# Optimization experiments

Measured on AMD Instinct MI355X. Metric: run time of the kernel, lower is better.

## Reference

```python
import jax, jax.numpy as jnp
import numpy as np

B, T, D, H = 64, 512, 1024, 1024


def setup_inputs() -> dict:
    key = jax.random.key(0)
    k1, k2, k3, k4, k5 = jax.random.split(key, 5)
    return {
        "c0": jax.random.normal(k1, (B, H), jnp.float32),
        "h0": jax.random.normal(k2, (B, H), jnp.float32),
        "x": jax.random.normal(k3, (B, T, D), jnp.float32),
        "Wi": jax.random.normal(k4, (D, 4 * H), jnp.float32) * 0.02,
        "Wh": jax.random.normal(k5, (H, 4 * H), jnp.float32) * 0.02,
        "b": jnp.zeros((4 * H,), jnp.float32),
    }


def reference(c0, h0, x, Wi, Wh, b):
    # flax OptimizedLSTMCell: fused gates = x @ Wi (no bias) + h @ Wh + b,
    # split into i, f, g, o; carry = (c, h).
    def step(carry, xt):
        c, h = carry
        gates = xt @ Wi + h @ Wh + b  # [B, 4H]
        i, f, g, o = jnp.split(gates, 4, axis=-1)
        new_c = jax.nn.sigmoid(f) * c + jax.nn.sigmoid(i) * jnp.tanh(g)
        new_h = jax.nn.sigmoid(o) * jnp.tanh(new_c)
        return (new_c, new_h), new_h

    # scan over time axis (original uses in_axes=1/out_axes=1)
    (cT, hT), ys = jax.lax.scan(step, (c0, h0), jnp.swapaxes(x, 0, 1))
    return cT, hT, jnp.swapaxes(ys, 0, 1)  # final carry + [B, T, H] outputs
```

## Files before the change

### kernel.cpp

```cpp
#include <hip/hip_runtime.h>

#define B_ 64
#define T_ 512
#define D_ 1024
#define H_ 1024
#define NG_ 4096

typedef __attribute__((ext_vector_type(8))) short short8v;
typedef __attribute__((ext_vector_type(4))) float f32x4;

static __device__ inline unsigned short f2bf(float f) {
  unsigned u = __float_as_uint(f);
  return (unsigned short)((u + 0x7fffu + ((u >> 16) & 1u)) >> 16);
}
static __device__ inline float bf2f(unsigned short s) {
  return __uint_as_float((unsigned)s << 16);
}

static __device__ inline float4 llc_load4(const float* p) {
  float4 r;
  asm volatile("global_load_dwordx4 %0, %1, off sc0 sc1" : "=v"(r) : "v"(p));
  return r;
}
static __device__ inline void llc_store1(float* p, float v) {
  asm volatile("global_store_dword %0, %1, off sc0 sc1" :: "v"(p), "v"(v) : "memory");
}
static __device__ inline void llc_store_u16(unsigned short* p, unsigned v) {
  asm volatile("global_store_short %0, %1, off sc0 sc1" :: "v"(p), "v"(v) : "memory");
}
#define VMWAIT(N)                                          \
  asm volatile("s_waitcnt vmcnt(" #N ")" ::: "memory");    \
  __builtin_amdgcn_sched_barrier(0);

__global__ __launch_bounds__(256) void k_trans_h_fwd(const float* __restrict__ h,
                                                     float* __restrict__ hT) {
  int idx = blockIdx.x * 256 + threadIdx.x;
  int b = idx & 63;
  int k = idx >> 6;
  hT[idx] = h[b * H_ + k];
}
__global__ __launch_bounds__(256) void k_trans_h_back(const float* __restrict__ hT,
                                                      float* __restrict__ h) {
  int idx = blockIdx.x * 256 + threadIdx.x;
  int k = idx & (H_ - 1);
  int b = idx >> 10;
  h[idx] = hT[k * 64 + b];
}

__global__ __launch_bounds__(256) void k_init_hfrag(const float* __restrict__ h0,
                                                    unsigned short* __restrict__ hf) {
  const int idx = blockIdx.x * 256 + threadIdx.x;
  const int j = idx & 7;
  const int l = (idx >> 3) & 63;
  const int bt = (idx >> 9) & 3;
  const int kt = idx >> 11;
  const int b = bt * 16 + (l & 15);
  const int k = kt * 32 + ((l >> 4) << 3) + j;
  hf[idx] = f2bf(h0[b * H_ + k]);
}

__global__ __launch_bounds__(256) void k_h_final(const float* __restrict__ ys,
                                                 float* __restrict__ h) {
  const int idx = blockIdx.x * 256 + threadIdx.x;
  const int b = idx >> 10;
  const int k = idx & 1023;
  h[idx] = ys[(size_t)b * (T_ * H_) + (size_t)(T_ - 1) * H_ + k];
}

__global__ __launch_bounds__(256) void k_prep_w(const float* __restrict__ Wi,
                                                short8v* __restrict__ wh,
                                                short8v* __restrict__ wl) {
  const int idx = blockIdx.x * 256 + threadIdx.x;
  const int l = idx & 63;
  const int kt = (idx >> 6) & 31;
  const int nt = idx >> 11;
  const int n = nt * 16 + (l & 15);
  const int k = kt * 32 + ((l >> 4) << 3);
  short8v h, lo;
#pragma unroll
  for (int j = 0; j < 8; ++j) {
    const float v = Wi[(size_t)(k + j) * NG_ + n];
    const unsigned short bh = f2bf(v);
    h[j] = (short)bh;
    lo[j] = (short)f2bf(v - bf2f(bh));
  }
  wh[idx] = h;
  wl[idx] = lo;
}

__global__ __launch_bounds__(256) void k_prep_x(const float* __restrict__ x,
                                                short8v* __restrict__ xh,
                                                short8v* __restrict__ xl,
                                                int t0) {
  const int idx = blockIdx.x * 256 + threadIdx.x;
  const int l = idx & 63;
  const int bt = (idx >> 6) & 3;
  const int kt = (idx >> 8) & 31;
  const int tt = idx >> 13;
  const int b = bt * 16 + (l & 15);
  const int k = kt * 32 + ((l >> 4) << 3);
  const float* p = x + ((size_t)b * T_ + (t0 + tt)) * D_ + k;
  const float4 f0 = *(const float4*)p;
  const float4 f1 = *(const float4*)(p + 4);
  const float v[8] = {f0.x, f0.y, f0.z, f0.w, f1.x, f1.y, f1.z, f1.w};
  short8v h, lo;
#pragma unroll
  for (int j = 0; j < 8; ++j) {
    const unsigned short bh = f2bf(v[j]);
    h[j] = (short)bh;
    lo[j] = (short)f2bf(v[j] - bf2f(bh));
  }
  xh[idx] = h;
  xl[idx] = lo;
}

__global__ __launch_bounds__(512, 2) void k_fused(
    const float* __restrict__ Wh,
    const short8v* __restrict__ xh, const short8v* __restrict__ xl,
    const short8v* __restrict__ wh, const short8v* __restrict__ wl,
    const float* __restrict__ bias,
    float* __restrict__ gx,
    unsigned short* __restrict__ hfA, unsigned short* __restrict__ hfB,
    float* __restrict__ c_state,
    float* __restrict__ ys,
    unsigned* __restrict__ bar,
    int t0, int tc) {
  extern __shared__ char smemc[];

  const int tid = threadIdx.x;
  const int l = tid & 63;
  const int w = tid >> 6;
  const int bid = blockIdx.x;
  unsigned* done = bar + 512;

  if (bid >= 128) {
    const int gi = bid - 128;
    const int oct = gi & 7;
    const int nt0 = oct * 32 + w * 4;
    for (int j = gi; j < tc * 8; j += 128) {
      const int tt = j >> 3;
      f32x4 acc[4][4];
#pragma unroll
      for (int i = 0; i < 4; ++i)
#pragma unroll
        for (int q = 0; q < 4; ++q) acc[i][q] = (f32x4){0.f, 0.f, 0.f, 0.f};

#pragma unroll 2
      for (int kt = 0; kt < 32; ++kt) {
        short8v ah[4], al[4], bh[4], bl[4];
#pragma unroll
        for (int bt = 0; bt < 4; ++bt) {
          const size_t ix = ((size_t)(tt * 32 + kt) * 4 + bt) * 64 + l;
          ah[bt] = xh[ix];
          al[bt] = xl[ix];
        }
#pragma unroll
        for (int q = 0; q < 4; ++q) {
          const size_t ix = ((size_t)(nt0 + q) * 32 + kt) * 64 + l;
          bh[q] = wh[ix];
          bl[q] = wl[ix];
        }
#pragma unroll
        for (int bt = 0; bt < 4; ++bt)
#pragma unroll
          for (int q = 0; q < 4; ++q) {
            acc[bt][q] = __builtin_amdgcn_mfma_f32_16x16x32_bf16(ah[bt], bh[q], acc[bt][q], 0, 0, 0);
            acc[bt][q] = __builtin_amdgcn_mfma_f32_16x16x32_bf16(al[bt], bh[q], acc[bt][q], 0, 0, 0);
            acc[bt][q] = __builtin_amdgcn_mfma_f32_16x16x32_bf16(ah[bt], bl[q], acc[bt][q], 0, 0, 0);
          }
      }

#pragma unroll
      for (int q = 0; q < 4; ++q) {
        const int n = (nt0 + q) * 16 + (l & 15);
        const int g = n >> 10;
        const int cb = (n & 1023) >> 2;
        const int c = n & 3;
        const float bv = bias[n];
#pragma unroll
        for (int bt = 0; bt < 4; ++bt)
#pragma unroll
          for (int r = 0; r < 4; ++r) {
            const int b = bt * 16 + (l >> 4) * 4 + r;
            llc_store1(gx + (((size_t)tt * 256 + cb) * 64 + b) * 16 + c * 4 + g,
                       acc[bt][q][r] + bv);
          }
      }
      asm volatile("s_waitcnt vmcnt(0)" ::: "memory");
      __syncthreads();
      if (tid == 0)
        __hip_atomic_fetch_add(&done[t0 + tt], 1u, __ATOMIC_RELAXED,
                               __HIP_MEMORY_SCOPE_AGENT);
    }
    return;
  }

  short8v* wldsh = (short8v*)smemc;
  short8v* wldsl = wldsh + 4096;
  float* red = (float*)(wldsl + 4096);

  const int bt = w & 3;
  const int kt0 = (w >> 2) * 16;
  const int hbase = bid * 8;

  for (int idx = tid; idx < 4096; idx += 512) {
    const int ct = idx >> 11;
    const int rem = idx & 2047;
    const int kt = rem >> 6;
    const int ll = rem & 63;
    const int cc = ll & 15;
    const int gc = ct * 16 + cc;
    const int c = gc >> 2, g = gc & 3;
    const int kb = kt * 32 + ((ll >> 4) << 3);
    short8v hi, lo;
#pragma unroll
    for (int j = 0; j < 8; ++j) {
      const float v = Wh[(size_t)(kb + j) * NG_ + g * H_ + hbase + c];
      const unsigned short bh = f2bf(v);
      hi[j] = (short)bh;
      lo[j] = (short)f2bf(v - bf2f(bh));
    }
    wldsh[idx] = hi;
    wldsl[idx] = lo;
  }

  const int eb = tid >> 3;
  const int c8 = tid & 7;
  const int hcol = hbase + c8;
  const size_t sOff = (((size_t)((hcol >> 5) * 4 + (eb >> 4)) * 64 +
                        ((((hcol & 31) >> 3) << 4) | (eb & 15))) * 8 + (hcol & 7));
  const int cbq = bid * 2 + (c8 >> 2);
  const int ebt = eb >> 4;
  const int erb = eb & 15;
  const int err_ = erb & 3;
  const int elrow = (erb >> 2) << 4;
  const int ect = c8 >> 2;

  float c_reg = c_state[eb * H_ + hcol];

  if (tid == 0) {
    while (__hip_atomic_load(&done[t0], __ATOMIC_RELAXED, __HIP_MEMORY_SCOPE_AGENT) < 8u)
      __builtin_amdgcn_s_sleep(1);
  }
  __syncthreads();

  for (int tt = 0; tt < tc; ++tt) {
    const int t = t0 + tt;
    const unsigned short* __restrict__ hf_in = (t & 1) ? hfB : hfA;
    unsigned short* __restrict__ hf_out = (t & 1) ? hfA : hfB;

    float4 gxv = llc_load4(gx + (((size_t)tt * 256 + cbq) * 64 + eb) * 16 + (c8 & 3) * 4);
    float4 aq[16];
#pragma unroll
    for (int q = 0; q < 16; ++q)
      aq[q] = llc_load4((const float*)(hf_in + (((size_t)(kt0 + q) * 4 + bt) * 64 + l) * 8));

    f32x4 acc0 = (f32x4){0.f, 0.f, 0.f, 0.f};
    f32x4 acc1 = (f32x4){0.f, 0.f, 0.f, 0.f};

#define STEPQ(Q, VM)                                                        \
    { const short8v bh0 = wldsh[(kt0 + (Q)) * 64 + l];                      \
      const short8v bl0 = wldsl[(kt0 + (Q)) * 64 + l];                      \
      const short8v bh1 = wldsh[2048 + (kt0 + (Q)) * 64 + l];               \
      const short8v bl1 = wldsl[2048 + (kt0 + (Q)) * 64 + l];               \
      VMWAIT(VM)                                                            \
      const short8v av = __builtin_bit_cast(short8v, aq[Q]);                \
      acc0 = __builtin_amdgcn_mfma_f32_16x16x32_bf16(av, bh0, acc0, 0, 0, 0); \
      acc0 = __builtin_amdgcn_mfma_f32_16x16x32_bf16(av, bl0, acc0, 0, 0, 0); \
      acc1 = __builtin_amdgcn_mfma_f32_16x16x32_bf16(av, bh1, acc1, 0, 0, 0); \
      acc1 = __builtin_amdgcn_mfma_f32_16x16x32_bf16(av, bl1, acc1, 0, 0, 0); }
    STEPQ(0, 15)  STEPQ(1, 14)  STEPQ(2, 13)  STEPQ(3, 12)
    STEPQ(4, 11)  STEPQ(5, 10)  STEPQ(6, 9)   STEPQ(7, 8)
    STEPQ(8, 7)   STEPQ(9, 6)   STEPQ(10, 5)  STEPQ(11, 4)
    STEPQ(12, 3)  STEPQ(13, 2)  STEPQ(14, 1)  STEPQ(15, 0)
#undef STEPQ

#pragma unroll
    for (int r = 0; r < 4; ++r) {
      red[((w * 2 + 0) * 64 + l) * 4 + r] = acc0[r];
      red[((w * 2 + 1) * 64 + l) * 4 + r] = acc1[r];
    }
    __syncthreads();

    {
      const float* gp = &gxv.x;
      float v[4];
#pragma unroll
      for (int g = 0; g < 4; ++g) {
        const int cc = (c8 & 3) * 4 + g;
        const int lp = elrow | cc;
        v[g] = gp[g] +
               red[(((0 * 4 + ebt) * 2 + ect) * 64 + lp) * 4 + err_] +
               red[(((1 * 4 + ebt) * 2 + ect) * 64 + lp) * 4 + err_];
      }
      const float si = 1.f / (1.f + expf(-v[0]));
      const float sf = 1.f / (1.f + expf(-v[1]));
      const float gt = tanhf(v[2]);
      const float so = 1.f / (1.f + expf(-v[3]));
      const float cn = sf * c_reg + si * gt;
      const float hn = so * tanhf(cn);
      c_reg = cn;
      llc_store_u16(hf_out + sOff, (unsigned)f2bf(hn));
      ys[(size_t)eb * (T_ * H_) + (size_t)t * H_ + hcol] = hn;
    }

    asm volatile("s_waitcnt vmcnt(0)" ::: "memory");
    __syncthreads();
    if (tid == 0) {
      __hip_atomic_fetch_add(&bar[(bid & 7) << 5], 1u,
                             __ATOMIC_RELAXED, __HIP_MEMORY_SCOPE_AGENT);
      const unsigned tgt = (unsigned)(t + 1);
      if (bid == 0) {
        unsigned s;
        do {
          s = 0;
#pragma unroll
          for (int i = 0; i < 8; ++i)
            s += __hip_atomic_load(&bar[i << 5], __ATOMIC_RELAXED,
                                   __HIP_MEMORY_SCOPE_AGENT);
          if (s < 128u * tgt) __builtin_amdgcn_s_sleep(1);
        } while (s < 128u * tgt);
        __hip_atomic_store(&bar[256], tgt, __ATOMIC_RELAXED,
                           __HIP_MEMORY_SCOPE_AGENT);
      } else {
        while (__hip_atomic_load(&bar[256], __ATOMIC_RELAXED,
                                 __HIP_MEMORY_SCOPE_AGENT) < tgt)
          __builtin_amdgcn_s_sleep(1);
      }
      if (tt + 1 < tc) {
        while (__hip_atomic_load(&done[t + 1], __ATOMIC_RELAXED,
                                 __HIP_MEMORY_SCOPE_AGENT) < 8u)
          __builtin_amdgcn_s_sleep(1);
      }
    }
    __syncthreads();
  }

  c_state[eb * H_ + hcol] = c_reg;
}

#define FMA16F(V, W0, W1, W2, W3)               \
  acc[0][0] = fmaf((V), (W0).x, acc[0][0]);     \
  acc[1][0] = fmaf((V), (W0).y, acc[1][0]);     \
  acc[2][0] = fmaf((V), (W0).z, acc[2][0]);     \
  acc[3][0] = fmaf((V), (W0).w, acc[3][0]);     \
  acc[0][1] = fmaf((V), (W1).x, acc[0][1]);     \
  acc[1][1] = fmaf((V), (W1).y, acc[1][1]);     \
  acc[2][1] = fmaf((V), (W1).z, acc[2][1]);     \
  acc[3][1] = fmaf((V), (W1).w, acc[3][1]);     \
  acc[0][2] = fmaf((V), (W2).x, acc[0][2]);     \
  acc[1][2] = fmaf((V), (W2).y, acc[1][2]);     \
  acc[2][2] = fmaf((V), (W2).z, acc[2][2]);     \
  acc[3][2] = fmaf((V), (W2).w, acc[3][2]);     \
  acc[0][3] = fmaf((V), (W3).x, acc[0][3]);     \
  acc[1][3] = fmaf((V), (W3).y, acc[1][3]);     \
  acc[2][3] = fmaf((V), (W3).z, acc[2][3]);     \
  acc[3][3] = fmaf((V), (W3).w, acc[3][3]);

__global__ __launch_bounds__(512, 2) void k_lstm_step_fused(
    const float* __restrict__ xsrc, const float* __restrict__ Wi,
    const float* __restrict__ Wh, const float* __restrict__ bias,
    const float* __restrict__ hT_in, float* __restrict__ hT_out,
    float* __restrict__ c_state, float* __restrict__ ys_t) {
  __shared__ float red[8 * 64 * 17];
  const int tid = threadIdx.x;
  const int lane = tid & 63;
  const int w = tid >> 6;
  const int hbase = blockIdx.x * 4;
  float acc[4][4];
#pragma unroll
  for (int c = 0; c < 4; ++c)
#pragma unroll
    for (int g = 0; g < 4; ++g) acc[c][g] = 0.f;
  const int k0 = w * 128;
#pragma unroll 2
  for (int k = k0; k < k0 + 128; ++k) {
    const float hv = hT_in[k * 64 + lane];
    const float xv = xsrc[(size_t)lane * (T_ * D_) + k];
    const float4 wh0 = *(const float4*)(Wh + (size_t)k * NG_ + 0 * H_ + hbase);
    const float4 wh1 = *(const float4*)(Wh + (size_t)k * NG_ + 1 * H_ + hbase);
    const float4 wh2 = *(const float4*)(Wh + (size_t)k * NG_ + 2 * H_ + hbase);
    const float4 wh3 = *(const float4*)(Wh + (size_t)k * NG_ + 3 * H_ + hbase);
    FMA16F(hv, wh0, wh1, wh2, wh3)
    const float4 wi0 = *(const float4*)(Wi + (size_t)k * NG_ + 0 * H_ + hbase);
    const float4 wi1 = *(const float4*)(Wi + (size_t)k * NG_ + 1 * H_ + hbase);
    const float4 wi2 = *(const float4*)(Wi + (size_t)k * NG_ + 2 * H_ + hbase);
    const float4 wi3 = *(const float4*)(Wi + (size_t)k * NG_ + 3 * H_ + hbase);
    FMA16F(xv, wi0, wi1, wi2, wi3)
  }
#pragma unroll
  for (int c = 0; c < 4; ++c)
#pragma unroll
    for (int g = 0; g < 4; ++g) red[(w * 64 + lane) * 17 + c * 4 + g] = acc[c][g];
  __syncthreads();
  if (tid < 256) {
    const int b = tid >> 2;
    const int c = tid & 3;
    const int h = hbase + c;
    float v[4];
#pragma unroll
    for (int g = 0; g < 4; ++g) {
      float s = bias[g * H_ + h];
#pragma unroll
      for (int ww = 0; ww < 8; ++ww) s += red[(ww * 64 + b) * 17 + c * 4 + g];
      v[g] = s;
    }
    const float cold = c_state[b * H_ + h];
    const float si = 1.f / (1.f + expf(-v[0]));
    const float sf = 1.f / (1.f + expf(-v[1]));
    const float gt = tanhf(v[2]);
    const float so = 1.f / (1.f + expf(-v[3]));
    const float cn = sf * cold + si * gt;
    const float hn = so * tanhf(cn);
    c_state[b * H_ + h] = cn;
    hT_out[h * 64 + b] = hn;
    ys_t[(size_t)b * (T_ * H_) + h] = hn;
  }
}

extern "C" void kernel_launch(void* const* d_in, const int* in_sizes, int n_in,
                              void* d_out, int out_size, void* d_ws, size_t ws_size,
                              hipStream_t stream) {
  const float* c0   = (const float*)d_in[0];
  const float* h0   = (const float*)d_in[1];
  const float* x    = (const float*)d_in[2];
  const float* Wi   = (const float*)d_in[3];
  const float* Wh   = (const float*)d_in[4];
  const float* bias = (const float*)d_in[5];

  float* out     = (float*)d_out;
  float* c_state = out;
  float* h_final = out + B_ * H_;
  float* ys      = out + 2 * B_ * H_;

  const size_t hbytes = (size_t)B_ * H_ * sizeof(float);
  char* ws = (char*)d_ws;
  unsigned* bar = (unsigned*)ws;
  char* hbufA = ws + 8192;
  char* hbufB = hbufA + hbytes;
  const size_t wfrag_n = (size_t)256 * 32 * 64;
  short8v* wh = (short8v*)(hbufB + hbytes);
  short8v* wl = wh + wfrag_n;
  char* chunkbase = (char*)(wl + wfrag_n);

  const size_t xfrag_t = (size_t)32 * 4 * 64;
  const size_t per_t = 2 * xfrag_t * sizeof(short8v) + (size_t)256 * 64 * 16 * sizeof(float);
  const size_t fixed = (size_t)(chunkbase - ws);
  size_t avail = (ws_size > fixed) ? ws_size - fixed : 0;
  int Tc = (int)(avail / per_t);
  if (Tc > T_) Tc = T_;

  hipMemsetAsync(bar, 0, 8192, stream);
  hipMemcpyAsync(c_state, c0, hbytes, hipMemcpyDeviceToDevice, stream);

  if (Tc >= 1) {
    unsigned short* hfA = (unsigned short*)hbufA;
    unsigned short* hfB = (unsigned short*)hbufB;

    k_init_hfrag<<<256, 256, 0, stream>>>(h0, hfA);
    k_prep_w<<<2048, 256, 0, stream>>>(Wi, wh, wl);

    const unsigned smem = (4096 + 4096) * 16 + 4096 * 4;

    for (int t0 = 0; t0 < T_; t0 += Tc) {
      const int tc = (T_ - t0 < Tc) ? (T_ - t0) : Tc;
      short8v* xh = (short8v*)chunkbase;
      short8v* xl = xh + (size_t)tc * xfrag_t;
      float* gxbuf = (float*)(xl + (size_t)tc * xfrag_t);

      k_prep_x<<<tc * 32, 256, 0, stream>>>(x, xh, xl, t0);

      int t0v = t0, tcv = tc;
      void* args[] = {(void*)&Wh,  (void*)&xh,   (void*)&xl, (void*)&wh,
                      (void*)&wl,  (void*)&bias, (void*)&gxbuf,
                      (void*)&hfA, (void*)&hfB,  (void*)&c_state,
                      (void*)&ys,  (void*)&bar,  (void*)&t0v, (void*)&tcv};
      hipLaunchCooperativeKernel((void*)k_fused, dim3(256), dim3(512), args,
                                 smem, stream);
    }
    k_h_final<<<256, 256, 0, stream>>>(ys, h_final);
  } else {
    float* hA = (float*)hbufA;
    float* hB = (float*)hbufB;
    k_trans_h_fwd<<<B_ * H_ / 256, 256, 0, stream>>>(h0, hA);
    for (int t = 0; t < T_; ++t) {
      const float* hin = (t & 1) ? hB : hA;
      float* hout      = (t & 1) ? hA : hB;
      k_lstm_step_fused<<<256, 512, 0, stream>>>(
          x + (size_t)t * D_, Wi, Wh, bias, hin, hout, c_state,
          ys + (size_t)t * H_);
    }
    k_trans_h_back<<<B_ * H_ / 256, 256, 0, stream>>>(hA, h_final);
  }
}
```

Baseline: 2.978 ms.

## Drop split-bf16 compensation for input projection and flatten grid barrier

The input projection x@Wi now uses a single bf16 MFMA per tile instead of the three-term hi/lo split emulating fp32, and the low-part buffers and their prep work are removed. This cuts MFMA work and memory traffic in the producer blocks and lets more timesteps fit in each workspace chunk. The grid barrier also changes: every block polls the summed counters itself rather than waiting on a flag published by block 0, and a separate wavefront waits on the gx-ready flag. Dropping the compensation lowers the precision of the input gates, which risks tolerance failures.

```diff
diff --git a/kernel.cpp b/kernel.cpp
--- a/kernel.cpp
+++ b/kernel.cpp
@@ -68,29 +68,21 @@
 }
 
 __global__ __launch_bounds__(256) void k_prep_w(const float* __restrict__ Wi,
-                                                short8v* __restrict__ wh,
-                                                short8v* __restrict__ wl) {
+                                                short8v* __restrict__ wh) {
   const int idx = blockIdx.x * 256 + threadIdx.x;
   const int l = idx & 63;
   const int kt = (idx >> 6) & 31;
   const int nt = idx >> 11;
   const int n = nt * 16 + (l & 15);
   const int k = kt * 32 + ((l >> 4) << 3);
-  short8v h, lo;
-#pragma unroll
-  for (int j = 0; j < 8; ++j) {
-    const float v = Wi[(size_t)(k + j) * NG_ + n];
-    const unsigned short bh = f2bf(v);
-    h[j] = (short)bh;
-    lo[j] = (short)f2bf(v - bf2f(bh));
-  }
+  short8v h;
+#pragma unroll
+  for (int j = 0; j < 8; ++j) h[j] = (short)f2bf(Wi[(size_t)(k + j) * NG_ + n]);
   wh[idx] = h;
-  wl[idx] = lo;
 }
 
 __global__ __launch_bounds__(256) void k_prep_x(const float* __restrict__ x,
                                                 short8v* __restrict__ xh,
-                                                short8v* __restrict__ xl,
                                                 int t0) {
   const int idx = blockIdx.x * 256 + threadIdx.x;
   const int l = idx & 63;
@@ -103,21 +95,16 @@
   const float4 f0 = *(const float4*)p;
   const float4 f1 = *(const float4*)(p + 4);
   const float v[8] = {f0.x, f0.y, f0.z, f0.w, f1.x, f1.y, f1.z, f1.w};
-  short8v h, lo;
-#pragma unroll
-  for (int j = 0; j < 8; ++j) {
-    const unsigned short bh = f2bf(v[j]);
-    h[j] = (short)bh;
-    lo[j] = (short)f2bf(v[j] - bf2f(bh));
-  }
+  short8v h;
+#pragma unroll
+  for (int j = 0; j < 8; ++j) h[j] = (short)f2bf(v[j]);
   xh[idx] = h;
-  xl[idx] = lo;
 }
 
 __global__ __launch_bounds__(512, 2) void k_fused(
     const float* __restrict__ Wh,
-    const short8v* __restrict__ xh, const short8v* __restrict__ xl,
-    const short8v* __restrict__ wh, const short8v* __restrict__ wl,
+    const short8v* __restrict__ xh,
+    const short8v* __restrict__ wh,
     const float* __restrict__ bias,
     float* __restrict__ gx,
     unsigned short* __restrict__ hfA, unsigned short* __restrict__ hfB,
@@ -147,27 +134,18 @@
 
 #pragma unroll 2
       for (int kt = 0; kt < 32; ++kt) {
-        short8v ah[4], al[4], bh[4], bl[4];
-#pragma unroll
-        for (int bt = 0; bt < 4; ++bt) {
-          const size_t ix = ((size_t)(tt * 32 + kt) * 4 + bt) * 64 + l;
-          ah[bt] = xh[ix];
-          al[bt] = xl[ix];
-        }
-#pragma unroll
-        for (int q = 0; q < 4; ++q) {
-          const size_t ix = ((size_t)(nt0 + q) * 32 + kt) * 64 + l;
-          bh[q] = wh[ix];
-          bl[q] = wl[ix];
-        }
+        short8v ah[4], bh[4];
 #pragma unroll
         for (int bt = 0; bt < 4; ++bt)
-#pragma unroll
-          for (int q = 0; q < 4; ++q) {
+          ah[bt] = xh[((size_t)(tt * 32 + kt) * 4 + bt) * 64 + l];
+#pragma unroll
+        for (int q = 0; q < 4; ++q)
+          bh[q] = wh[((size_t)(nt0 + q) * 32 + kt) * 64 + l];
+#pragma unroll
+        for (int bt = 0; bt < 4; ++bt)
+#pragma unroll
+          for (int q = 0; q < 4; ++q)
             acc[bt][q] = __builtin_amdgcn_mfma_f32_16x16x32_bf16(ah[bt], bh[q], acc[bt][q], 0, 0, 0);
-            acc[bt][q] = __builtin_amdgcn_mfma_f32_16x16x32_bf16(al[bt], bh[q], acc[bt][q], 0, 0, 0);
-            acc[bt][q] = __builtin_amdgcn_mfma_f32_16x16x32_bf16(ah[bt], bl[q], acc[bt][q], 0, 0, 0);
-          }
       }
 
 #pragma unroll
@@ -309,29 +287,21 @@
     if (tid == 0) {
       __hip_atomic_fetch_add(&bar[(bid & 7) << 5], 1u,
                              __ATOMIC_RELAXED, __HIP_MEMORY_SCOPE_AGENT);
-      const unsigned tgt = (unsigned)(t + 1);
-      if (bid == 0) {
-        unsigned s;
-        do {
-          s = 0;
-#pragma unroll
-          for (int i = 0; i < 8; ++i)
-            s += __hip_atomic_load(&bar[i << 5], __ATOMIC_RELAXED,
-                                   __HIP_MEMORY_SCOPE_AGENT);
-          if (s < 128u * tgt) __builtin_amdgcn_s_sleep(1);
-        } while (s < 128u * tgt);
-        __hip_atomic_store(&bar[256], tgt, __ATOMIC_RELAXED,
-                           __HIP_MEMORY_SCOPE_AGENT);
-      } else {
-        while (__hip_atomic_load(&bar[256], __ATOMIC_RELAXED,
-                                 __HIP_MEMORY_SCOPE_AGENT) < tgt)
-          __builtin_amdgcn_s_sleep(1);
-      }
-      if (tt + 1 < tc) {
-        while (__hip_atomic_load(&done[t + 1], __ATOMIC_RELAXED,
-                                 __HIP_MEMORY_SCOPE_AGENT) < 8u)
-          __builtin_amdgcn_s_sleep(1);
-      }
+      const unsigned tgt = 128u * (unsigned)(t + 1);
+      unsigned s;
+      do {
+        s = 0;
+#pragma unroll
+        for (int i = 0; i < 8; ++i)
+          s += __hip_atomic_load(&bar[i << 5], __ATOMIC_RELAXED,
+                                 __HIP_MEMORY_SCOPE_AGENT);
+        if (s < tgt) __builtin_amdgcn_s_sleep(1);
+      } while (s < tgt);
+    }
+    if (tid == 64 && tt + 1 < tc) {
+      while (__hip_atomic_load(&done[t + 1], __ATOMIC_RELAXED,
+                               __HIP_MEMORY_SCOPE_AGENT) < 8u)
+        __builtin_amdgcn_s_sleep(1);
     }
     __syncthreads();
   }
@@ -440,11 +410,10 @@
   char* hbufB = hbufA + hbytes;
   const size_t wfrag_n = (size_t)256 * 32 * 64;
   short8v* wh = (short8v*)(hbufB + hbytes);
-  short8v* wl = wh + wfrag_n;
-  char* chunkbase = (char*)(wl + wfrag_n);
+  char* chunkbase = (char*)(wh + wfrag_n);
 
   const size_t xfrag_t = (size_t)32 * 4 * 64;
-  const size_t per_t = 2 * xfrag_t * sizeof(short8v) + (size_t)256 * 64 * 16 * sizeof(float);
+  const size_t per_t = xfrag_t * sizeof(short8v) + (size_t)256 * 64 * 16 * sizeof(float);
   const size_t fixed = (size_t)(chunkbase - ws);
   size_t avail = (ws_size > fixed) ? ws_size - fixed : 0;
   int Tc = (int)(avail / per_t);
@@ -458,21 +427,20 @@
     unsigned short* hfB = (unsigned short*)hbufB;
 
     k_init_hfrag<<<256, 256, 0, stream>>>(h0, hfA);
-    k_prep_w<<<2048, 256, 0, stream>>>(Wi, wh, wl);
+    k_prep_w<<<2048, 256, 0, stream>>>(Wi, wh);
 
     const unsigned smem = (4096 + 4096) * 16 + 4096 * 4;
 
     for (int t0 = 0; t0 < T_; t0 += Tc) {
       const int tc = (T_ - t0 < Tc) ? (T_ - t0) : Tc;
       short8v* xh = (short8v*)chunkbase;
-      short8v* xl = xh + (size_t)tc * xfrag_t;
-      float* gxbuf = (float*)(xl + (size_t)tc * xfrag_t);
-
-      k_prep_x<<<tc * 32, 256, 0, stream>>>(x, xh, xl, t0);
+      float* gxbuf = (float*)(xh + (size_t)tc * xfrag_t);
+
+      k_prep_x<<<tc * 32, 256, 0, stream>>>(x, xh, t0);
 
       int t0v = t0, tcv = tc;
-      void* args[] = {(void*)&Wh,  (void*)&xh,   (void*)&xl, (void*)&wh,
-                      (void*)&wl,  (void*)&bias, (void*)&gxbuf,
+      void* args[] = {(void*)&Wh,  (void*)&xh,   (void*)&wh,
+                      (void*)&bias, (void*)&gxbuf,
                       (void*)&hfA, (void*)&hfB,  (void*)&c_state,
                       (void*)&ys,  (void*)&bar,  (void*)&t0v, (void*)&tcv};
       hipLaunchCooperativeKernel((void*)k_fused, dim3(256), dim3(512), args,
```

New measurement: 2.808 ms. 1.06x faster.
